# Kernel tuning notes

Measured on AMD Instinct MI355X. Metric: run time of the kernel, lower is better.

The kernel has to match this reference:

```python
import jax, jax.numpy as jnp
import numpy as np

SPATIAL_SHAPES = ((128, 128), (64, 64), (32, 32), (16, 16))  # (h, w) per level
N_HEADS, N_LEVELS, N_POINTS, D_MODEL = 8, 4, 4, 256


def setup_inputs() -> dict:
    key = jax.random.key(0)
    ks = jax.random.split(key, 10)
    bs, nq, nk = 4, 300, 17
    inp = {
        'query': jax.random.normal(ks[0], (bs, nq * nk, D_MODEL), jnp.float32),
        'reference_points': jax.random.uniform(ks[1], (bs, nq, N_LEVELS, nk, 2), jnp.float32),
    }
    for l, (h, w) in enumerate(SPATIAL_SHAPES):
        inp[f'value{l}'] = jax.random.normal(ks[2 + l], (bs * N_HEADS, D_MODEL // N_HEADS, h * w), jnp.float32)
    inp['W_off'] = jax.random.normal(ks[6], (N_HEADS * N_LEVELS * N_POINTS * 2, D_MODEL), jnp.float32) * 0.02
    inp['b_off'] = jax.random.normal(ks[7], (N_HEADS * N_LEVELS * N_POINTS * 2,), jnp.float32) * 0.5
    inp['W_attn'] = jax.random.normal(ks[8], (N_HEADS * N_LEVELS * N_POINTS, D_MODEL), jnp.float32) * 0.02
    inp['b_attn'] = jax.random.normal(ks[9], (N_HEADS * N_LEVELS * N_POINTS,), jnp.float32) * 0.02
    return inp


def _bilinear_sample(v, grid, h, w):
    # v: (N, C, h*w); grid: (N, P, 2) normalized to [-1, 1] (x, y).
    # F.grid_sample bilinear, padding_mode='zeros', align_corners=False.
    x = (grid[..., 0] + 1.0) * 0.5 * w - 0.5
    y = (grid[..., 1] + 1.0) * 0.5 * h - 0.5
    x0 = jnp.floor(x)
    y0 = jnp.floor(y)
    wx1, wy1 = x - x0, y - y0
    wx0, wy0 = 1.0 - wx1, 1.0 - wy1
    x0i, y0i = x0.astype(jnp.int32), y0.astype(jnp.int32)
    out = 0.0
    for xi, yi, wgt in ((x0i, y0i, wx0 * wy0), (x0i + 1, y0i, wx1 * wy0),
                        (x0i, y0i + 1, wx0 * wy1), (x0i + 1, y0i + 1, wx1 * wy1)):
        valid = (xi >= 0) & (xi < w) & (yi >= 0) & (yi < h)
        idx = jnp.clip(yi, 0, h - 1) * w + jnp.clip(xi, 0, w - 1)       # (N, P)
        g = jnp.take_along_axis(v, idx[:, None, :], axis=2)              # (N, C, P)
        out = out + g * (wgt * valid.astype(v.dtype))[:, None, :]
    return out


def reference(query, reference_points, value0, value1, value2, value3, W_off, b_off, W_attn, b_attn):
    bs, len_q, _ = query.shape
    hd = D_MODEL // N_HEADS
    values = (value0, value1, value2, value3)

    off = (query @ W_off.T + b_off).reshape(bs, len_q, N_HEADS, N_LEVELS, N_POINTS, 2)
    attn = (query @ W_attn.T + b_attn).reshape(bs, len_q, N_HEADS, N_LEVELS * N_POINTS)
    attn = jax.nn.softmax(attn, axis=-1)

    # (bs, nq, L, nk, 2) -> transpose(2,3) -> flatten(1,2) -> (bs, len_q, L, 2)
    rp = jnp.transpose(reference_points, (0, 1, 3, 2, 4)).reshape(bs, len_q, N_LEVELS, 2)
    # normalizer: spatial (h, w) flipped -> (w, h)
    norm = jnp.array([[w, h] for (h, w) in SPATIAL_SHAPES], dtype=query.dtype).reshape(1, 1, 1, N_LEVELS, 1, 2)
    loc = rp[:, :, None, :, None, :] + off / norm                         # (bs, len_q, H, L, P, 2)

    grids = 2.0 * loc - 1.0
    grids = jnp.transpose(grids, (0, 2, 1, 3, 4, 5)).reshape(bs * N_HEADS, len_q, N_LEVELS, N_POINTS, 2)

    sampled = []
    for l, (h, w) in enumerate(SPATIAL_SHAPES):
        g = grids[:, :, l].reshape(bs * N_HEADS, len_q * N_POINTS, 2)
        s = _bilinear_sample(values[l], g, h, w)                          # (bs*H, hd, len_q*P)
        sampled.append(s.reshape(bs * N_HEADS, hd, len_q, N_POINTS))
    sampled = jnp.concatenate(sampled, axis=-1)                           # (bs*H, hd, len_q, L*P)

    attn_r = jnp.transpose(attn, (0, 2, 1, 3)).reshape(bs * N_HEADS, 1, len_q, N_LEVELS * N_POINTS)
    out = (sampled * attn_r).sum(-1).reshape(bs, D_MODEL, len_q)
    return jnp.transpose(out, (0, 2, 1))                                  # (bs, len_q, d_model)
```

## Files before the change

### kernel.cpp

```cpp
#include <hip/hip_runtime.h>
#include <math.h>

#define BS        4
#define NQ        300
#define NK        17
#define LEN_Q     5100
#define N_HEADS   8
#define N_LEVELS  4
#define N_POINTS  4
#define D_MODEL   256
#define HD        32

#define LB0 0
#define LB1 16777216
#define LB2 20971520
#define LB3 22020096
#define VT_TOTAL 22282240

typedef __attribute__((ext_vector_type(8))) short bf16x8;
typedef __attribute__((ext_vector_type(4))) float f32x4;

__device__ __forceinline__ unsigned short f2bf(float x) {
    unsigned u = __float_as_uint(x);
    unsigned r = (u + 0x7fffu + ((u >> 16) & 1u)) >> 16;
    return (unsigned short)r;
}
__device__ __forceinline__ float bf2f(unsigned short s) {
    return __uint_as_float((unsigned)s << 16);
}
__device__ __forceinline__ bf16x8 cvt8(const float* __restrict__ p) {
    float4 a = *(const float4*)p;
    float4 b = *(const float4*)(p + 4);
    bf16x8 r;
    r[0] = f2bf(a.x); r[1] = f2bf(a.y); r[2] = f2bf(a.z); r[3] = f2bf(a.w);
    r[4] = f2bf(b.x); r[5] = f2bf(b.y); r[6] = f2bf(b.z); r[7] = f2bf(b.w);
    return r;
}

__global__ __launch_bounds__(256) void transpose_bf16_kernel(
    const float* __restrict__ v0, const float* __restrict__ v1,
    const float* __restrict__ v2, const float* __restrict__ v3,
    unsigned short* __restrict__ vt)
{
    __shared__ float t[32][33];
    int bx = blockIdx.x;
    int n  = blockIdx.y;

    const float* in; int S; size_t ob; int tile;
    if (bx < 512)      { in = v0; S = 16384; ob = LB0; tile = bx; }
    else if (bx < 640) { in = v1; S = 4096;  ob = LB1; tile = bx - 512; }
    else if (bx < 672) { in = v2; S = 1024;  ob = LB2; tile = bx - 640; }
    else               { in = v3; S = 256;   ob = LB3; tile = bx - 672; }

    int s0 = tile * 32;
    const float* pin = in + (size_t)n * 32 * S;
    #pragma unroll
    for (int c = threadIdx.y; c < 32; c += 8) {
        t[c][threadIdx.x] = pin[(size_t)c * S + s0 + threadIdx.x];
    }
    __syncthreads();
    unsigned short* pout = vt + ob + (size_t)n * S * 32;
    #pragma unroll
    for (int r = threadIdx.y; r < 32; r += 8) {
        pout[(size_t)(s0 + r) * 32 + threadIdx.x] = f2bf(t[threadIdx.x][r]);
    }
}

__global__ __launch_bounds__(256) void proj_gemm_mfma(
    const float* __restrict__ Q,
    const float* __restrict__ Woff, const float* __restrict__ boff,
    const float* __restrict__ Wattn, const float* __restrict__ battn,
    float* __restrict__ P, int M)
{
    int tid  = threadIdx.x;
    int wave = tid >> 6;
    int lane = tid & 63;
    int bm = blockIdx.y * 64;
    int bn = blockIdx.x * 128;
    int wm = (wave & 1) * 32;
    int wn = (wave >> 1) * 64;
    int lr = lane & 15;
    int lk = (lane >> 4) * 8;

    f32x4 acc[2][4] = {};
    for (int k0 = 0; k0 < 256; k0 += 32) {
        bf16x8 afrag[2], bfrag[4];
        #pragma unroll
        for (int i = 0; i < 2; ++i) {
            int row = bm + wm + i * 16 + lr;
            row = row < M ? row : M - 1;
            afrag[i] = cvt8(Q + (size_t)row * 256 + k0 + lk);
        }
        #pragma unroll
        for (int j = 0; j < 4; ++j) {
            int n = bn + wn + j * 16 + lr;
            const float* wp = (n < 256) ? (Woff + (size_t)n * 256)
                                        : (Wattn + (size_t)(n - 256) * 256);
            bfrag[j] = cvt8(wp + k0 + lk);
        }
        #pragma unroll
        for (int i = 0; i < 2; ++i)
            #pragma unroll
            for (int j = 0; j < 4; ++j)
                acc[i][j] = __builtin_amdgcn_mfma_f32_16x16x32_bf16(
                    afrag[i], bfrag[j], acc[i][j], 0, 0, 0);
    }

    #pragma unroll
    for (int i = 0; i < 2; ++i) {
        int mbase = bm + wm + i * 16 + (lane >> 4) * 4;
        #pragma unroll
        for (int j = 0; j < 4; ++j) {
            int n = bn + wn + j * 16 + (lane & 15);
            float bias = (n < 256) ? boff[n] : battn[n - 256];
            #pragma unroll
            for (int r = 0; r < 4; ++r) {
                int row = mbase + r;
                if (row < M) P[(size_t)row * 384 + n] = acc[i][j][r] + bias;
            }
        }
    }
}

__global__ __launch_bounds__(256) void ms_deform_kernel(
    const float* __restrict__ rp,
    const float* __restrict__ proj,
    const unsigned short* __restrict__ vt,
    float* __restrict__ out)
{
    int bq = blockIdx.x;
    int b  = bq / LEN_Q;
    int q  = bq - b * LEN_Q;
    int qi = q / NK;
    int ki = q - qi * NK;

    __shared__ int   s_iw[128][12];
    __shared__ float s_attn[128];
    __shared__ float4 s_red[256];

    int tid = threadIdx.x;
    const float* prow = proj + (size_t)bq * 384;

    if (tid < 128) {
        float g = prow[256 + tid];
        float mx = g;
        mx = fmaxf(mx, __shfl_xor(mx, 1, 16));
        mx = fmaxf(mx, __shfl_xor(mx, 2, 16));
        mx = fmaxf(mx, __shfl_xor(mx, 4, 16));
        mx = fmaxf(mx, __shfl_xor(mx, 8, 16));
        float e = __expf(g - mx);
        float s = e;
        s += __shfl_xor(s, 1, 16);
        s += __shfl_xor(s, 2, 16);
        s += __shfl_xor(s, 4, 16);
        s += __shfl_xor(s, 8, 16);
        s_attn[tid] = e / s;
    }
    __syncthreads();

    if (tid < 128) {
        int h  = tid & 7;
        int lp = tid >> 3;
        int l  = lp >> 2;
        int p  = lp & 3;
        int Wl = 128 >> l;
        float ww = (float)Wl;

        size_t rbase = ((((size_t)b * NQ + qi) * N_LEVELS + l) * NK + ki) * 2;
        float rx = rp[rbase + 0];
        float ry = rp[rbase + 1];
        int oj = ((h * N_LEVELS + l) * N_POINTS + p) * 2;
        float ox = prow[oj], oy = prow[oj + 1];
        float x = (rx + ox / ww) * ww - 0.5f;
        float y = (ry + oy / ww) * ww - 0.5f;
        float x0f = floorf(x), y0f = floorf(y);
        float wx1 = x - x0f, wy1 = y - y0f;
        float wx0 = 1.f - wx1, wy0 = 1.f - wy1;
        int x0 = (int)x0f, y0 = (int)y0f;

        float a = s_attn[h * 16 + lp];

        #pragma unroll
        for (int corner = 0; corner < 4; ++corner) {
            int xi = x0 + (corner & 1);
            int yi = y0 + (corner >> 1);
            float wgt = ((corner & 1) ? wx1 : wx0) * ((corner >> 1) ? wy1 : wy0);
            bool valid = (xi >= 0) && (xi < Wl) && (yi >= 0) && (yi < Wl);
            int2 iw;
            iw.x = valid ? (yi * Wl + xi) * HD : 0;
            iw.y = __float_as_int(valid ? wgt * a : 0.f);
            *(int2*)&s_iw[tid][corner * 2] = iw;
        }
    }
    __syncthreads();

    int l  = tid >> 6;
    int h  = (tid >> 3) & 7;
    int c4 = tid & 7;
    int n  = b * N_HEADS + h;
    const size_t lb[4]  = {LB0, LB1, LB2, LB3};
    const int    Ssz[4] = {16384, 4096, 1024, 256};

    const unsigned short* vbase = vt + lb[l] + (size_t)n * Ssz[l] * HD + c4 * 4;
    int rb = l * 32 + h;

    float4 acc = make_float4(0.f, 0.f, 0.f, 0.f);
    #pragma unroll
    for (int p = 0; p < 4; ++p) {
        int4 A  = *(const int4*)&s_iw[rb + p * 8][0];
        int4 Bv = *(const int4*)&s_iw[rb + p * 8][4];
        ushort4 u0 = *(const ushort4*)(vbase + A.x);
        ushort4 u1 = *(const ushort4*)(vbase + A.z);
        ushort4 u2 = *(const ushort4*)(vbase + Bv.x);
        ushort4 u3 = *(const ushort4*)(vbase + Bv.z);
        float w0 = __int_as_float(A.y);
        float w1 = __int_as_float(A.w);
        float w2 = __int_as_float(Bv.y);
        float w3 = __int_as_float(Bv.w);
        acc.x += w0 * bf2f(u0.x) + w1 * bf2f(u1.x) + w2 * bf2f(u2.x) + w3 * bf2f(u3.x);
        acc.y += w0 * bf2f(u0.y) + w1 * bf2f(u1.y) + w2 * bf2f(u2.y) + w3 * bf2f(u3.y);
        acc.z += w0 * bf2f(u0.z) + w1 * bf2f(u1.z) + w2 * bf2f(u2.z) + w3 * bf2f(u3.z);
        acc.w += w0 * bf2f(u0.w) + w1 * bf2f(u1.w) + w2 * bf2f(u2.w) + w3 * bf2f(u3.w);
    }

    s_red[tid] = acc;
    __syncthreads();
    if (tid < 64) {
        float4 a0 = s_red[tid];
        float4 a1 = s_red[tid + 64];
        float4 a2 = s_red[tid + 128];
        float4 a3 = s_red[tid + 192];
        float4 o;
        o.x = a0.x + a1.x + a2.x + a3.x;
        o.y = a0.y + a1.y + a2.y + a3.y;
        o.z = a0.z + a1.z + a2.z + a3.z;
        o.w = a0.w + a1.w + a2.w + a3.w;
        *(float4*)(out + (size_t)bq * 256 + tid * 4) = o;
    }
}

extern "C" void kernel_launch(void* const* d_in, const int* in_sizes, int n_in,
                              void* d_out, int out_size, void* d_ws, size_t ws_size,
                              hipStream_t stream)
{
    const float* query = (const float*)d_in[0];
    const float* refp  = (const float*)d_in[1];
    const float* v0    = (const float*)d_in[2];
    const float* v1    = (const float*)d_in[3];
    const float* v2    = (const float*)d_in[4];
    const float* v3    = (const float*)d_in[5];
    const float* Woff  = (const float*)d_in[6];
    const float* boff  = (const float*)d_in[7];
    const float* Wattn = (const float*)d_in[8];
    const float* battn = (const float*)d_in[9];
    float* out = (float*)d_out;
    unsigned short* vt = (unsigned short*)d_ws;
    float* proj = (float*)(vt + VT_TOTAL);

    transpose_bf16_kernel<<<dim3(680, 32), dim3(32, 8), 0, stream>>>(
        v0, v1, v2, v3, vt);

    int M = BS * LEN_Q;
    proj_gemm_mfma<<<dim3(3, (M + 63) / 64), 256, 0, stream>>>(
        query, Woff, boff, Wattn, battn, proj, M);

    ms_deform_kernel<<<M, 256, 0, stream>>>(refp, proj, vt, out);
}
```

Before: 131.9 us.

## Remap deform-attn blocks to (query chunk, batch, head) for gather locality

After: 129.1 us. 1.02x faster.

```diff
diff --git a/kernel.cpp b/kernel.cpp
--- a/kernel.cpp
+++ b/kernel.cpp
@@ -128,21 +128,27 @@
     const unsigned short* __restrict__ vt,
     float* __restrict__ out)
 {
-    int bq = blockIdx.x;
-    int b  = bq / LEN_Q;
-    int q  = bq - b * LEN_Q;
-    int qi = q / NK;
-    int ki = q - qi * NK;
-
-    __shared__ int   s_iw[128][12];
-    __shared__ float s_attn[128];
+    int bid = blockIdx.x;
+    int h   = bid & 7;
+    int b   = (bid >> 3) & 3;
+    int qc  = bid >> 5;
+    int q0  = qc * 8;
+
+    __shared__ int s_iw[1552];
     __shared__ float4 s_red[256];
 
     int tid = threadIdx.x;
-    const float* prow = proj + (size_t)bq * 384;
 
     if (tid < 128) {
-        float g = prow[256 + tid];
+        int q8 = tid >> 4;
+        int lp = tid & 15;
+        int l  = lp >> 2;
+        int p  = lp & 3;
+        int q  = q0 + q8;
+        int qq = q < LEN_Q ? q : LEN_Q - 1;
+        const float* prow = proj + (size_t)(b * LEN_Q + qq) * 384;
+
+        float g = prow[256 + h * 16 + lp];
         float mx = g;
         mx = fmaxf(mx, __shfl_xor(mx, 1, 16));
         mx = fmaxf(mx, __shfl_xor(mx, 2, 16));
@@ -154,22 +160,16 @@
         s += __shfl_xor(s, 2, 16);
         s += __shfl_xor(s, 4, 16);
         s += __shfl_xor(s, 8, 16);
-        s_attn[tid] = e / s;
-    }
-    __syncthreads();
-
-    if (tid < 128) {
-        int h  = tid & 7;
-        int lp = tid >> 3;
-        int l  = lp >> 2;
-        int p  = lp & 3;
+        float a = (q < LEN_Q) ? (e / s) : 0.f;
+
         int Wl = 128 >> l;
         float ww = (float)Wl;
-
+        int qi = qq / NK;
+        int ki = qq - qi * NK;
         size_t rbase = ((((size_t)b * NQ + qi) * N_LEVELS + l) * NK + ki) * 2;
         float rx = rp[rbase + 0];
         float ry = rp[rbase + 1];
-        int oj = ((h * N_LEVELS + l) * N_POINTS + p) * 2;
+        int oj = (h * 16 + lp) * 2;
         float ox = prow[oj], oy = prow[oj + 1];
         float x = (rx + ox / ww) * ww - 0.5f;
         float y = (ry + oy / ww) * ww - 0.5f;
@@ -178,8 +178,7 @@
         float wx0 = 1.f - wx1, wy0 = 1.f - wy1;
         int x0 = (int)x0f, y0 = (int)y0f;
 
-        float a = s_attn[h * 16 + lp];
-
+        int* wrow = s_iw + (q8 >> 1) * 388 + (p * 8 + l * 2 + (q8 & 1)) * 12;
         #pragma unroll
         for (int corner = 0; corner < 4; ++corner) {
             int xi = x0 + (corner & 1);
@@ -189,26 +188,27 @@
             int2 iw;
             iw.x = valid ? (yi * Wl + xi) * HD : 0;
             iw.y = __float_as_int(valid ? wgt * a : 0.f);
-            *(int2*)&s_iw[tid][corner * 2] = iw;
+            *(int2*)(wrow + corner * 2) = iw;
         }
     }
     __syncthreads();
 
     int l  = tid >> 6;
-    int h  = (tid >> 3) & 7;
+    int q8 = (tid >> 3) & 7;
     int c4 = tid & 7;
     int n  = b * N_HEADS + h;
     const size_t lb[4]  = {LB0, LB1, LB2, LB3};
     const int    Ssz[4] = {16384, 4096, 1024, 256};
 
     const unsigned short* vbase = vt + lb[l] + (size_t)n * Ssz[l] * HD + c4 * 4;
-    int rb = l * 32 + h;
+    const int* rrow0 = s_iw + (q8 >> 1) * 388 + (l * 2 + (q8 & 1)) * 12;
 
     float4 acc = make_float4(0.f, 0.f, 0.f, 0.f);
     #pragma unroll
     for (int p = 0; p < 4; ++p) {
-        int4 A  = *(const int4*)&s_iw[rb + p * 8][0];
-        int4 Bv = *(const int4*)&s_iw[rb + p * 8][4];
+        const int* rr = rrow0 + p * 96;
+        int4 A  = *(const int4*)rr;
+        int4 Bv = *(const int4*)(rr + 4);
         ushort4 u0 = *(const ushort4*)(vbase + A.x);
         ushort4 u1 = *(const ushort4*)(vbase + A.z);
         ushort4 u2 = *(const ushort4*)(vbase + Bv.x);
@@ -226,16 +226,21 @@
     s_red[tid] = acc;
     __syncthreads();
     if (tid < 64) {
-        float4 a0 = s_red[tid];
-        float4 a1 = s_red[tid + 64];
-        float4 a2 = s_red[tid + 128];
-        float4 a3 = s_red[tid + 192];
+        int q8o = tid >> 3;
+        int c4o = tid & 7;
+        int base = q8o * 8 + c4o;
+        float4 a0 = s_red[base];
+        float4 a1 = s_red[base + 64];
+        float4 a2 = s_red[base + 128];
+        float4 a3 = s_red[base + 192];
         float4 o;
         o.x = a0.x + a1.x + a2.x + a3.x;
         o.y = a0.y + a1.y + a2.y + a3.y;
         o.z = a0.z + a1.z + a2.z + a3.z;
         o.w = a0.w + a1.w + a2.w + a3.w;
-        *(float4*)(out + (size_t)bq * 256 + tid * 4) = o;
+        int q = q0 + q8o;
+        if (q < LEN_Q)
+            *(float4*)(out + (size_t)(b * LEN_Q + q) * 256 + h * 32 + c4o * 4) = o;
     }
 }
 
@@ -264,5 +269,5 @@
     proj_gemm_mfma<<<dim3(3, (M + 63) / 64), 256, 0, stream>>>(
         query, Woff, boff, Wattn, battn, proj, M);
 
-    ms_deform_kernel<<<M, 256, 0, stream>>>(refp, proj, vt, out);
-}
+    ms_deform_kernel<<<638 * 32, 256, 0, stream>>>(refp, proj, vt, out);
+}
```
